# Kernel tuning notes

Hardware: AMD Instinct MI355X
Metric: run time of the kernel (lower is better)

Reference implementation:

```python
import jax, jax.numpy as jnp
import numpy as np
import math

D, H, NQP, NKP = 512, 8, 4, 4
DH = D // H
OUT_DIM = D + H * NKP * 3  # 608


def setup_inputs() -> dict:
    key = jax.random.key(0)
    ks = jax.random.split(key, 12)
    B, L = 2, 1024
    s = jax.random.normal(ks[0], (B, L, D), dtype=jnp.float32)
    R = jax.random.normal(ks[1], (B, L, 3, 3), dtype=jnp.float32)
    tr = jax.random.normal(ks[2], (B, L, 3), dtype=jnp.float32)
    sc = 0.02
    Wq = jax.random.normal(ks[3], (D, D), dtype=jnp.float32) * sc
    Wk = jax.random.normal(ks[4], (D, D), dtype=jnp.float32) * sc
    Wv = jax.random.normal(ks[5], (D, D), dtype=jnp.float32) * sc
    Wqp = jax.random.normal(ks[6], (D, H * NQP * 3), dtype=jnp.float32) * sc
    Wkp = jax.random.normal(ks[7], (D, H * NKP * 3), dtype=jnp.float32) * sc
    Wvp = jax.random.normal(ks[8], (D, H * NKP * 3), dtype=jnp.float32) * sc
    Wo = jax.random.normal(ks[9], (OUT_DIM, D), dtype=jnp.float32) * sc
    bo = jnp.zeros((D,), dtype=jnp.float32)
    gamma = jnp.ones((D,), dtype=jnp.float32)
    beta = jnp.zeros((D,), dtype=jnp.float32)
    w_C = jnp.full((H,), math.log(20.0), dtype=jnp.float32)
    return dict(s=s, R=R, tr=tr, Wq=Wq, Wk=Wk, Wv=Wv, Wqp=Wqp, Wkp=Wkp,
                Wvp=Wvp, Wo=Wo, bo=bo, gamma=gamma, beta=beta, w_C=w_C)


def _layernorm(x, gamma, beta, eps=1e-5):
    mu = jnp.mean(x, axis=-1, keepdims=True)
    var = jnp.var(x, axis=-1, keepdims=True)
    return (x - mu) * jax.lax.rsqrt(var + eps) * gamma + beta


def reference(s, R, tr, Wq, Wk, Wv, Wqp, Wkp, Wvp, Wo, bo, gamma, beta, w_C):
    B, L, _ = s.shape
    # scalar q/k/v: (B, L, H, dh)
    Q = (s @ Wq).reshape(B, L, H, DH)
    K = (s @ Wk).reshape(B, L, H, DH)
    V = (s @ Wv).reshape(B, L, H, DH)
    a_s = jnp.einsum('bihd,bjhd->bhij', Q, K) / math.sqrt(DH)
    # local points: (B, L, H, P, 3)
    Qp = (s @ Wqp).reshape(B, L, H, NQP, 3)
    Kp = (s @ Wkp).reshape(B, L, H, NKP, 3)
    Vp = (s @ Wvp).reshape(B, L, H, NKP, 3)
    tr_e = tr[:, :, None, None, :]
    to_global = lambda p: jnp.einsum('blxy,blhpy->blhpx', R, p) + tr_e
    Qp_g, Kp_g, Vp_g = to_global(Qp), to_global(Kp), to_global(Vp)
    # (B, H, L, P, 3)
    qh = jnp.transpose(Qp_g, (0, 2, 1, 3, 4))
    kh = jnp.transpose(Kp_g, (0, 2, 1, 3, 4))
    diff = qh[:, :, :, None] - kh[:, :, None]          # (B,H,L,L,P,3)
    sq_dist = jnp.sum(diff * diff, axis=(-2, -1))      # (B,H,L,L)
    wc = jax.nn.softplus(w_C)[None, :, None, None]
    attn = jax.nn.softmax(a_s - 0.5 * wc * sq_dist, axis=-1)
    out_s = jnp.einsum('bhij,bjhd->bihd', attn, V).reshape(B, L, D)
    Vp_agg = jnp.einsum('bhij,bjhpc->bihpc', attn, Vp_g)  # (B,L,H,P,3)
    # global -> local: R^T (p - tr)
    Vp_local = jnp.einsum('blyx,blhpy->blhpx', R, Vp_agg - tr_e)
    out_p = Vp_local.reshape(B, L, H * NKP * 3)
    out = jnp.concatenate([out_s, out_p], axis=-1) @ Wo + bo
    return _layernorm(s + out, gamma, beta)
```

## Files before the change

### kernel.cpp

```cpp
#include <hip/hip_runtime.h>
#include <hip/hip_fp16.h>
#include <math.h>

typedef _Float16 f16;
typedef _Float16 f16x8 __attribute__((ext_vector_type(8)));
typedef _Float16 f16x4v __attribute__((ext_vector_type(4)));
typedef float f32x4 __attribute__((ext_vector_type(4)));

#define BATCH   2
#define LSEQ    1024
#define BLTOT   2048
#define DMODEL  512
#define NHEAD   8
#define PDIM    1824
#define AW      96
#define ODIM    608
#define NSPLIT  2

__global__ __launch_bounds__(256)
void convert_s_kernel(const float* __restrict__ s, f16* __restrict__ out)
{
    const int i = blockIdx.x * 256 + threadIdx.x;
    float4 v = ((const float4*)s)[i];
    f16x4v o = { (f16)v.x, (f16)v.y, (f16)v.z, (f16)v.w };
    ((f16x4v*)out)[i] = o;
}

__global__ __launch_bounds__(256)
void transpose_wall_kernel(const float* __restrict__ Wq, const float* __restrict__ Wk,
                           const float* __restrict__ Wv, const float* __restrict__ Wqp,
                           const float* __restrict__ Wkp, const float* __restrict__ Wvp,
                           f16* __restrict__ WT)
{
    const int n0 = blockIdx.x * 32, k0 = blockIdx.y * 32;
    const int t = threadIdx.x;
    const float* src; int ld, nc0;
    if      (n0 < 512)  { src = Wq;  ld = 512; nc0 = n0; }
    else if (n0 < 1024) { src = Wk;  ld = 512; nc0 = n0 - 512; }
    else if (n0 < 1536) { src = Wv;  ld = 512; nc0 = n0 - 1024; }
    else if (n0 < 1632) { src = Wqp; ld = 96;  nc0 = n0 - 1536; }
    else if (n0 < 1728) { src = Wkp; ld = 96;  nc0 = n0 - 1632; }
    else                { src = Wvp; ld = 96;  nc0 = n0 - 1728; }

    __shared__ float tile[32][33];
#pragma unroll
    for (int i = 0; i < 4; ++i) {
        const int idx = t + i * 256;
        const int kl = idx >> 5, nl = idx & 31;
        tile[kl][nl] = src[(long long)(k0 + kl) * ld + nc0 + nl];
    }
    __syncthreads();
#pragma unroll
    for (int i = 0; i < 4; ++i) {
        const int idx = t + i * 256;
        const int nl = idx >> 5, kl = idx & 31;
        WT[(long long)(n0 + nl) * 512 + k0 + kl] = (f16)tile[kl][nl];
    }
}

__global__ __launch_bounds__(256)
void transpose_wo_kernel(const float* __restrict__ Wo, f16* __restrict__ WT)
{
    const int n0 = blockIdx.x * 32, k0 = blockIdx.y * 32;
    const int t = threadIdx.x;
    __shared__ float tile[32][33];
#pragma unroll
    for (int i = 0; i < 4; ++i) {
        const int idx = t + i * 256;
        const int kl = idx >> 5, nl = idx & 31;
        tile[kl][nl] = Wo[(long long)(k0 + kl) * 512 + n0 + nl];
    }
    __syncthreads();
#pragma unroll
    for (int i = 0; i < 4; ++i) {
        const int idx = t + i * 256;
        const int nl = idx >> 5, kl = idx & 31;
        WT[(long long)(n0 + nl) * 608 + k0 + kl] = (f16)tile[kl][nl];
    }
}

template<int BN, bool OUT16>
__global__ __launch_bounds__(256)
void gemm2_kernel(const f16* __restrict__ A, const f16* __restrict__ Bt,
                  void* __restrict__ Cout, int K, int ldc)
{
    constexpr int BCH = (BN * 4 + 255) / 256;
    __shared__ f16 As[2][64][40];
    __shared__ f16 Bs[2][BN][40];
    const int t = threadIdx.x;
    const int w = t >> 6, lane = t & 63, l15 = lane & 15, lhi = lane >> 4;
    const int row0 = blockIdx.y * 64, col0 = blockIdx.x * BN;
    const int ar = t >> 2, ac = t & 3;

    f32x4 acc[BN / 16];
#pragma unroll
    for (int n = 0; n < BN / 16; ++n) acc[n] = (f32x4){0.f, 0.f, 0.f, 0.f};

    const int nsteps = K >> 5;

    f16x8 aR;
    f16x8 bR[BCH];
    aR = *(const f16x8*)&A[(long long)(row0 + ar) * K + ac * 8];
#pragma unroll
    for (int i = 0; i < BCH; ++i) {
        const int cid = t + i * 256;
        if (cid < BN * 4) {
            const int br = cid >> 2, bc = cid & 3;
            bR[i] = *(const f16x8*)&Bt[(long long)(col0 + br) * K + bc * 8];
        }
    }
    *(f16x8*)&As[0][ar][ac * 8] = aR;
#pragma unroll
    for (int i = 0; i < BCH; ++i) {
        const int cid = t + i * 256;
        if (cid < BN * 4) *(f16x8*)&Bs[0][cid >> 2][(cid & 3) * 8] = bR[i];
    }
    __syncthreads();

    for (int st = 0; st < nsteps; ++st) {
        const int cur = st & 1;
        if (st + 1 < nsteps) {
            const int k0 = (st + 1) << 5;
            aR = *(const f16x8*)&A[(long long)(row0 + ar) * K + k0 + ac * 8];
#pragma unroll
            for (int i = 0; i < BCH; ++i) {
                const int cid = t + i * 256;
                if (cid < BN * 4) {
                    const int br = cid >> 2, bc = cid & 3;
                    bR[i] = *(const f16x8*)&Bt[(long long)(col0 + br) * K + k0 + bc * 8];
                }
            }
        }
        f16x8 af = *(const f16x8*)&As[cur][w * 16 + l15][lhi * 8];
        f16x8 bf[BN / 16];
#pragma unroll
        for (int n = 0; n < BN / 16; ++n)
            bf[n] = *(const f16x8*)&Bs[cur][n * 16 + l15][lhi * 8];
#pragma unroll
        for (int n = 0; n < BN / 16; ++n)
            acc[n] = __builtin_amdgcn_mfma_f32_16x16x32_f16(af, bf[n], acc[n], 0, 0, 0);
        if (st + 1 < nsteps) {
            *(f16x8*)&As[cur ^ 1][ar][ac * 8] = aR;
#pragma unroll
            for (int i = 0; i < BCH; ++i) {
                const int cid = t + i * 256;
                if (cid < BN * 4) *(f16x8*)&Bs[cur ^ 1][cid >> 2][(cid & 3) * 8] = bR[i];
            }
        }
        __syncthreads();
    }

    const int row = row0 + w * 16 + lhi * 4;
#pragma unroll
    for (int n = 0; n < BN / 16; ++n) {
        const int col = col0 + n * 16 + l15;
#pragma unroll
        for (int r = 0; r < 4; ++r) {
            if (OUT16) ((f16*)Cout)[(long long)(row + r) * ldc + col] = (f16)acc[n][r];
            else       ((float*)Cout)[(long long)(row + r) * ldc + col] = acc[n][r];
        }
    }
}

__global__ __launch_bounds__(256)
void build_aug_kernel(const f16* __restrict__ P, const float* __restrict__ Rm,
                      const float* __restrict__ tr, const float* __restrict__ wC,
                      f16* __restrict__ QA, f16* __restrict__ KA,
                      f16* __restrict__ VC, float* __restrict__ KOFF)
{
    const int bl = blockIdx.x;
    const int b = bl >> 10, l = bl & 1023;
    const int t = threadIdx.x;

    __shared__ float g[3][NHEAD][4][3];
    __shared__ float Rloc[9], trloc[3], wcl[NHEAD];

    if (t < 9) Rloc[t] = Rm[(long long)bl * 9 + t];
    if (t < 3) trloc[t] = tr[(long long)bl * 3 + t];
    if (t < NHEAD) { float x = wC[t]; wcl[t] = log1pf(expf(x)); }
    __syncthreads();

    const f16* Prow = P + (long long)bl * PDIM;

    if (t < 96) {
        const int proj = t / 32, tpl = t % 32, h = tpl >> 2, p = tpl & 3;
        const f16* src = Prow + 1536 + proj * 96 + h * 12 + p * 3;
        const float x = (float)src[0], y = (float)src[1], z = (float)src[2];
        g[proj][h][p][0] = Rloc[0]*x + Rloc[1]*y + Rloc[2]*z + trloc[0];
        g[proj][h][p][1] = Rloc[3]*x + Rloc[4]*y + Rloc[5]*z + trloc[1];
        g[proj][h][p][2] = Rloc[6]*x + Rloc[7]*y + Rloc[8]*z + trloc[2];
    }
    __syncthreads();

    if (t < NHEAD) {
        float s2 = 0.f;
#pragma unroll
        for (int p = 0; p < 4; ++p)
#pragma unroll
            for (int c = 0; c < 3; ++c) { float v = g[1][t][p][c]; s2 += v * v; }
        KOFF[(long long)(b * NHEAD + t) * LSEQ + l] = 0.5f * wcl[t] * s2;
    }

    for (int w = t; w < NHEAD * AW; w += 256) {
        const int h = w / AW, col = w % AW;
        const long long ro = ((long long)(b * NHEAD + h) * LSEQ + l) * AW;
        const float wc = wcl[h];
        float qv = 0.f, kv = 0.f, vv = 0.f;
        if (col < 64) {
            qv = (float)Prow[h * 64 + col] * 0.125f;
            kv = (float)Prow[512 + h * 64 + col];
            vv = (float)Prow[1024 + h * 64 + col];
        } else if (col < 76) {
            const int pc = col - 64, p = pc / 3, c = pc % 3;
            qv = wc * g[0][h][p][c];
            kv = g[1][h][p][c];
            vv = g[2][h][p][c];
        }
        QA[ro + col] = (f16)qv;
        KA[ro + col] = (f16)kv;
        VC[ro + col] = (f16)vv;
    }
}

__global__ __launch_bounds__(256)
void transpose_vct_kernel(const f16* __restrict__ VC, f16* __restrict__ VCT)
{
    const int bh = blockIdx.y, l0 = blockIdx.x * 128;
    const int t = threadIdx.x;
    __shared__ f16 tile[128][104];
#pragma unroll
    for (int i = 0; i < 6; ++i) {
        const int cid = t + i * 256;
        const int r = cid / 12, c = cid - r * 12;
        *(f16x8*)&tile[r][c * 8] =
            *(const f16x8*)&VC[((long long)bh * LSEQ + l0 + r) * AW + c * 8];
    }
    __syncthreads();
#pragma unroll
    for (int i = 0; i < 6; ++i) {
        const int cid = t + i * 256;
        const int r = cid >> 4, lg = cid & 15;
        f16x8 v;
#pragma unroll
        for (int j = 0; j < 8; ++j) v[j] = tile[lg * 8 + j][r];
        *(f16x8*)&VCT[((long long)bh * AW + r) * LSEQ + l0 + lg * 8] = v;
    }
}

__global__ __launch_bounds__(256)
void attn_kernel(const f16* __restrict__ QA, const f16* __restrict__ KA,
                 const f16* __restrict__ VCT, const float* __restrict__ KOFF,
                 float* __restrict__ OCp, float2* __restrict__ ML)
{
    const int bh = blockIdx.y;
    const int q0 = blockIdx.x * 64;
    const int z  = blockIdx.z;
    const int t = threadIdx.x;
    const int w = t >> 6, lane = t & 63, l15 = lane & 15, lhi = lane >> 4;

    __shared__ f16 Ks[128][104];
    __shared__ f16 Vs[96][136];
    __shared__ f16 Ps[64][136];

    const f16* qbase = QA + ((long long)bh * LSEQ + q0 + w * 16 + l15) * AW;
    f16x8 qf[3];
#pragma unroll
    for (int ks = 0; ks < 3; ++ks)
        qf[ks] = *(const f16x8*)(qbase + ks * 32 + lhi * 8);

    f32x4 Oacc[6];
#pragma unroll
    for (int nv = 0; nv < 6; ++nv) Oacc[nv] = (f32x4){0.f, 0.f, 0.f, 0.f};
    float M[4], L[4];
#pragma unroll
    for (int r = 0; r < 4; ++r) { M[r] = -1e30f; L[r] = 0.f; }

    const f16* kgbase = KA + (long long)bh * LSEQ * AW;
    const f16* vgbase = VCT + (long long)bh * AW * LSEQ;
    const float* koffb = KOFF + (long long)bh * LSEQ;

    const int kvbeg = z * (LSEQ / NSPLIT);
    const int kvend = kvbeg + LSEQ / NSPLIT;

    for (int kv0 = kvbeg; kv0 < kvend; kv0 += 128) {
#pragma unroll
        for (int i = 0; i < 6; ++i) {
            const int cid = t + i * 256;
            const int r = cid / 12, c = cid - r * 12;
            *(f16x8*)&Ks[r][c * 8] = *(const f16x8*)(kgbase + (long long)(kv0 + r) * AW + c * 8);
        }
#pragma unroll
        for (int i = 0; i < 6; ++i) {
            const int cid = t + i * 256;
            const int r = cid >> 4, c = cid & 15;
            *(f16x8*)&Vs[r][c * 8] = *(const f16x8*)(vgbase + (long long)r * LSEQ + kv0 + c * 8);
        }
        __syncthreads();

        f32x4 sc[8];
#pragma unroll
        for (int n = 0; n < 8; ++n) sc[n] = (f32x4){0.f, 0.f, 0.f, 0.f};
        __builtin_amdgcn_s_setprio(1);
#pragma unroll
        for (int n = 0; n < 8; ++n)
#pragma unroll
            for (int ks = 0; ks < 3; ++ks) {
                f16x8 kb = *(const f16x8*)&Ks[n * 16 + l15][ks * 32 + lhi * 8];
                sc[n] = __builtin_amdgcn_mfma_f32_16x16x32_f16(qf[ks], kb, sc[n], 0, 0, 0);
            }
        __builtin_amdgcn_s_setprio(0);
#pragma unroll
        for (int n = 0; n < 8; ++n) {
            const float ko = koffb[kv0 + n * 16 + l15];
#pragma unroll
            for (int r = 0; r < 4; ++r) sc[n][r] -= ko;
        }
        float sscale[4];
#pragma unroll
        for (int r = 0; r < 4; ++r) {
            float mr = sc[0][r];
#pragma unroll
            for (int n = 1; n < 8; ++n) mr = fmaxf(mr, sc[n][r]);
#pragma unroll
            for (int off = 1; off < 16; off <<= 1) mr = fmaxf(mr, __shfl_xor(mr, off));
            const float nm = fmaxf(M[r], mr);
            sscale[r] = __expf(M[r] - nm);
            M[r] = nm;
        }
        float rsum[4] = {0.f, 0.f, 0.f, 0.f};
#pragma unroll
        for (int n = 0; n < 8; ++n)
#pragma unroll
            for (int r = 0; r < 4; ++r) {
                const float p = __expf(sc[n][r] - M[r]);
                sc[n][r] = p;
                rsum[r] += p;
            }
#pragma unroll
        for (int r = 0; r < 4; ++r) {
            float s = rsum[r];
#pragma unroll
            for (int off = 1; off < 16; off <<= 1) s += __shfl_xor(s, off);
            L[r] = L[r] * sscale[r] + s;
        }
#pragma unroll
        for (int nv = 0; nv < 6; ++nv)
#pragma unroll
            for (int r = 0; r < 4; ++r) Oacc[nv][r] *= sscale[r];

#pragma unroll
        for (int n = 0; n < 8; ++n)
#pragma unroll
            for (int r = 0; r < 4; ++r)
                Ps[w * 16 + lhi * 4 + r][n * 16 + l15] = (f16)sc[n][r];

        f16x8 pa[4];
#pragma unroll
        for (int ks = 0; ks < 4; ++ks)
            pa[ks] = *(const f16x8*)&Ps[w * 16 + l15][ks * 32 + lhi * 8];
        __builtin_amdgcn_s_setprio(1);
#pragma unroll
        for (int nv = 0; nv < 6; ++nv)
#pragma unroll
            for (int ks = 0; ks < 4; ++ks) {
                f16x8 vb = *(const f16x8*)&Vs[nv * 16 + l15][ks * 32 + lhi * 8];
                Oacc[nv] = __builtin_amdgcn_mfma_f32_16x16x32_f16(pa[ks], vb, Oacc[nv], 0, 0, 0);
            }
        __builtin_amdgcn_s_setprio(0);
        __syncthreads();
    }

    float* obase = OCp + (((long long)(z * 16 + bh) * LSEQ) + q0 + w * 16 + lhi * 4) * AW;
#pragma unroll
    for (int nv = 0; nv < 6; ++nv)
#pragma unroll
        for (int r = 0; r < 4; ++r)
            obase[r * AW + nv * 16 + l15] = Oacc[nv][r];
    if (l15 == 0) {
#pragma unroll
        for (int r = 0; r < 4; ++r)
            ML[(long long)(z * 16 + bh) * LSEQ + q0 + w * 16 + lhi * 4 + r] =
                make_float2(M[r], L[r]);
    }
}

__global__ __launch_bounds__(256)
void combine_concat_kernel(const float* __restrict__ OCp, const float2* __restrict__ ML,
                           const float* __restrict__ Rm, const float* __restrict__ tr,
                           f16* __restrict__ CC)
{
    const int bl = blockIdx.x;
    const int b = bl >> 10, l = bl & 1023;
    const int t = threadIdx.x;

    __shared__ float w1[8], w2[8];
    __shared__ float o[8][AW];
    __shared__ float Rloc[9], trloc[3];
    if (t < 9) Rloc[t] = Rm[(long long)bl * 9 + t];
    if (t < 3) trloc[t] = tr[(long long)bl * 3 + t];
    if (t < 8) {
        const int bh = b * 8 + t;
        const float2 m1 = ML[(long long)bh * LSEQ + l];
        const float2 m2 = ML[(long long)(16 + bh) * LSEQ + l];
        const float mm = fmaxf(m1.x, m2.x);
        const float e1 = __expf(m1.x - mm), e2 = __expf(m2.x - mm);
        const float inv = 1.0f / (m1.y * e1 + m2.y * e2);
        w1[t] = e1 * inv; w2[t] = e2 * inv;
    }
    __syncthreads();
    for (int idx = t; idx < 8 * AW; idx += 256) {
        const int h = idx / AW, c = idx - h * AW;
        const float* p1 = OCp + ((long long)(b * 8 + h) * LSEQ + l) * AW;
        const float* p2 = OCp + ((long long)(16 + b * 8 + h) * LSEQ + l) * AW;
        o[h][c] = p1[c] * w1[h] + p2[c] * w2[h];
    }
    __syncthreads();

    f16* crow = CC + (long long)bl * ODIM;
    for (int c = t; c < DMODEL; c += 256) crow[c] = (f16)o[c >> 6][c & 63];
    if (t < 32) {
        const int h = t >> 2, p = t & 3;
        const float x = o[h][64 + p * 3 + 0] - trloc[0];
        const float y = o[h][64 + p * 3 + 1] - trloc[1];
        const float z = o[h][64 + p * 3 + 2] - trloc[2];
        crow[512 + h * 12 + p * 3 + 0] = (f16)(Rloc[0]*x + Rloc[3]*y + Rloc[6]*z);
        crow[512 + h * 12 + p * 3 + 1] = (f16)(Rloc[1]*x + Rloc[4]*y + Rloc[7]*z);
        crow[512 + h * 12 + p * 3 + 2] = (f16)(Rloc[2]*x + Rloc[5]*y + Rloc[8]*z);
    }
}

__global__ __launch_bounds__(256)
void residual_ln_kernel(const float* __restrict__ s, const float* __restrict__ Y,
                        const float* __restrict__ bo, const float* __restrict__ gamma,
                        const float* __restrict__ beta, float* __restrict__ out)
{
    const int bl = blockIdx.x;
    const int t = threadIdx.x;
    const float* srow = s + (long long)bl * DMODEL;
    const float* yrow = Y + (long long)bl * DMODEL;

    const float v0 = srow[t]       + yrow[t]       + bo[t];
    const float v1 = srow[t + 256] + yrow[t + 256] + bo[t + 256];

    float sum = v0 + v1, sq = v0 * v0 + v1 * v1;
#pragma unroll
    for (int o = 32; o > 0; o >>= 1) {
        sum += __shfl_xor(sum, o);
        sq  += __shfl_xor(sq,  o);
    }
    __shared__ float rs[4], rq[4];
    const int wid = t >> 6, lane = t & 63;
    if (lane == 0) { rs[wid] = sum; rq[wid] = sq; }
    __syncthreads();
    sum = rs[0] + rs[1] + rs[2] + rs[3];
    sq  = rq[0] + rq[1] + rq[2] + rq[3];

    const float mu  = sum * (1.0f / DMODEL);
    const float var = sq * (1.0f / DMODEL) - mu * mu;
    const float inv = rsqrtf(var + 1e-5f);

    out[(long long)bl * DMODEL + t]       = (v0 - mu) * inv * gamma[t]       + beta[t];
    out[(long long)bl * DMODEL + t + 256] = (v1 - mu) * inv * gamma[t + 256] + beta[t + 256];
}

extern "C" void kernel_launch(void* const* d_in, const int* in_sizes, int n_in,
                              void* d_out, int out_size, void* d_ws, size_t ws_size,
                              hipStream_t stream)
{
    const float* s    = (const float*)d_in[0];
    const float* R    = (const float*)d_in[1];
    const float* tr   = (const float*)d_in[2];
    const float* Wq   = (const float*)d_in[3];
    const float* Wk   = (const float*)d_in[4];
    const float* Wv   = (const float*)d_in[5];
    const float* Wqp  = (const float*)d_in[6];
    const float* Wkp  = (const float*)d_in[7];
    const float* Wvp  = (const float*)d_in[8];
    const float* Wo   = (const float*)d_in[9];
    const float* bo   = (const float*)d_in[10];
    const float* gam  = (const float*)d_in[11];
    const float* bet  = (const float*)d_in[12];
    const float* wC   = (const float*)d_in[13];
    float* out = (float*)d_out;

    f16* sH    = (f16*)d_ws;
    f16* WallT = sH + 1048576;
    f16* WoT   = WallT + 933888;
    f16* P     = WoT + 311296;
    f16* QA    = P + 3735552;
    f16* KA    = QA + 1572864;
    f16* VC    = KA + 1572864;
    f16* VCT   = VC + 1572864;
    float* KOFF = (float*)(VCT + 1572864);
    float* OCp  = KOFF + 16384;
    float2* ML  = (float2*)(OCp + 3145728);
    f16* CC     = (f16*)(ML + 32768);
    float* Y    = (float*)(CC + 1245184);

    const dim3 blk(256);

    convert_s_kernel<<<dim3(1024), blk, 0, stream>>>(s, sH);
    transpose_wall_kernel<<<dim3(57, 16), blk, 0, stream>>>(Wq, Wk, Wv, Wqp, Wkp, Wvp, WallT);
    transpose_wo_kernel<<<dim3(16, 19), blk, 0, stream>>>(Wo, WoT);

    gemm2_kernel<96, true><<<dim3(19, 32), blk, 0, stream>>>(sH, WallT, P, 512, 1824);

    build_aug_kernel<<<dim3(BLTOT), blk, 0, stream>>>(P, R, tr, wC, QA, KA, VC, KOFF);
    transpose_vct_kernel<<<dim3(8, 16), blk, 0, stream>>>(VC, VCT);

    attn_kernel<<<dim3(16, 16, NSPLIT), blk, 0, stream>>>(QA, KA, VCT, KOFF, OCp, ML);

    combine_concat_kernel<<<dim3(BLTOT), blk, 0, stream>>>(OCp, ML, R, tr, CC);

    gemm2_kernel<64, false><<<dim3(8, 32), blk, 0, stream>>>(CC, WoT, Y, 608, 512);

    residual_ln_kernel<<<dim3(BLTOT), blk, 0, stream>>>(s, Y, bo, gam, bet, out);
}
```

Before: 79.57 us.

## Merge prep kernels, fuse build and V transpose, prefetch KV, fp16 partials

Merges the s conversion and both weight transposes into one prep kernel. Replaces the per-row build_aug and separate V transpose with a per-(batch, head, 64-row) tile kernel that writes QA/KA with vector stores and VCT directly through shared memory. In attention, the next K/V tile is register-prefetched while the current tile is computed, launch_bounds is raised to 2 blocks per SM, and the split-KV partial outputs are stored as fp16. This removes launches and intermediate traffic, at the cost of more register pressure and lower precision in the partial outputs.

```diff
diff --git a/kernel.cpp b/kernel.cpp
--- a/kernel.cpp
+++ b/kernel.cpp
@@ -18,64 +18,65 @@
 #define NSPLIT  2
 
 __global__ __launch_bounds__(256)
-void convert_s_kernel(const float* __restrict__ s, f16* __restrict__ out)
-{
-    const int i = blockIdx.x * 256 + threadIdx.x;
-    float4 v = ((const float4*)s)[i];
-    f16x4v o = { (f16)v.x, (f16)v.y, (f16)v.z, (f16)v.w };
-    ((f16x4v*)out)[i] = o;
-}
-
-__global__ __launch_bounds__(256)
-void transpose_wall_kernel(const float* __restrict__ Wq, const float* __restrict__ Wk,
-                           const float* __restrict__ Wv, const float* __restrict__ Wqp,
-                           const float* __restrict__ Wkp, const float* __restrict__ Wvp,
-                           f16* __restrict__ WT)
-{
-    const int n0 = blockIdx.x * 32, k0 = blockIdx.y * 32;
-    const int t = threadIdx.x;
-    const float* src; int ld, nc0;
-    if      (n0 < 512)  { src = Wq;  ld = 512; nc0 = n0; }
-    else if (n0 < 1024) { src = Wk;  ld = 512; nc0 = n0 - 512; }
-    else if (n0 < 1536) { src = Wv;  ld = 512; nc0 = n0 - 1024; }
-    else if (n0 < 1632) { src = Wqp; ld = 96;  nc0 = n0 - 1536; }
-    else if (n0 < 1728) { src = Wkp; ld = 96;  nc0 = n0 - 1632; }
-    else                { src = Wvp; ld = 96;  nc0 = n0 - 1728; }
-
-    __shared__ float tile[32][33];
-#pragma unroll
-    for (int i = 0; i < 4; ++i) {
-        const int idx = t + i * 256;
-        const int kl = idx >> 5, nl = idx & 31;
-        tile[kl][nl] = src[(long long)(k0 + kl) * ld + nc0 + nl];
-    }
-    __syncthreads();
-#pragma unroll
-    for (int i = 0; i < 4; ++i) {
-        const int idx = t + i * 256;
-        const int nl = idx >> 5, kl = idx & 31;
-        WT[(long long)(n0 + nl) * 512 + k0 + kl] = (f16)tile[kl][nl];
-    }
-}
-
-__global__ __launch_bounds__(256)
-void transpose_wo_kernel(const float* __restrict__ Wo, f16* __restrict__ WT)
-{
-    const int n0 = blockIdx.x * 32, k0 = blockIdx.y * 32;
+void prep_kernel(const float* __restrict__ s,
+                 const float* __restrict__ Wq, const float* __restrict__ Wk,
+                 const float* __restrict__ Wv, const float* __restrict__ Wqp,
+                 const float* __restrict__ Wkp, const float* __restrict__ Wvp,
+                 const float* __restrict__ Wo,
+                 f16* __restrict__ sH, f16* __restrict__ WallT, f16* __restrict__ WoT)
+{
+    const int blk = blockIdx.x;
     const int t = threadIdx.x;
     __shared__ float tile[32][33];
-#pragma unroll
-    for (int i = 0; i < 4; ++i) {
-        const int idx = t + i * 256;
-        const int kl = idx >> 5, nl = idx & 31;
-        tile[kl][nl] = Wo[(long long)(k0 + kl) * 512 + n0 + nl];
-    }
-    __syncthreads();
-#pragma unroll
-    for (int i = 0; i < 4; ++i) {
-        const int idx = t + i * 256;
-        const int nl = idx >> 5, kl = idx & 31;
-        WT[(long long)(n0 + nl) * 608 + k0 + kl] = (f16)tile[kl][nl];
+
+    if (blk < 1024) {
+        const int i = blk * 256 + t;
+        float4 v = ((const float4*)s)[i];
+        f16x4v o = { (f16)v.x, (f16)v.y, (f16)v.z, (f16)v.w };
+        ((f16x4v*)sH)[i] = o;
+        return;
+    }
+    if (blk < 1936) {
+        const int idx = blk - 1024;
+        const int n0 = (idx % 57) * 32, k0 = (idx / 57) * 32;
+        const float* src; int ld, nc0;
+        if      (n0 < 512)  { src = Wq;  ld = 512; nc0 = n0; }
+        else if (n0 < 1024) { src = Wk;  ld = 512; nc0 = n0 - 512; }
+        else if (n0 < 1536) { src = Wv;  ld = 512; nc0 = n0 - 1024; }
+        else if (n0 < 1632) { src = Wqp; ld = 96;  nc0 = n0 - 1536; }
+        else if (n0 < 1728) { src = Wkp; ld = 96;  nc0 = n0 - 1632; }
+        else                { src = Wvp; ld = 96;  nc0 = n0 - 1728; }
+#pragma unroll
+        for (int i = 0; i < 4; ++i) {
+            const int idx2 = t + i * 256;
+            const int kl = idx2 >> 5, nl = idx2 & 31;
+            tile[kl][nl] = src[(long long)(k0 + kl) * ld + nc0 + nl];
+        }
+        __syncthreads();
+#pragma unroll
+        for (int i = 0; i < 4; ++i) {
+            const int idx2 = t + i * 256;
+            const int nl = idx2 >> 5, kl = idx2 & 31;
+            WallT[(long long)(n0 + nl) * 512 + k0 + kl] = (f16)tile[kl][nl];
+        }
+        return;
+    }
+    {
+        const int idx = blk - 1936;
+        const int n0 = (idx % 16) * 32, k0 = (idx / 16) * 32;
+#pragma unroll
+        for (int i = 0; i < 4; ++i) {
+            const int idx2 = t + i * 256;
+            const int kl = idx2 >> 5, nl = idx2 & 31;
+            tile[kl][nl] = Wo[(long long)(k0 + kl) * 512 + n0 + nl];
+        }
+        __syncthreads();
+#pragma unroll
+        for (int i = 0; i < 4; ++i) {
+            const int idx2 = t + i * 256;
+            const int nl = idx2 >> 5, kl = idx2 & 31;
+            WoT[(long long)(n0 + nl) * 608 + k0 + kl] = (f16)tile[kl][nl];
+        }
     }
 }
 
@@ -163,94 +164,108 @@
 }
 
 __global__ __launch_bounds__(256)
-void build_aug_kernel(const f16* __restrict__ P, const float* __restrict__ Rm,
-                      const float* __restrict__ tr, const float* __restrict__ wC,
-                      f16* __restrict__ QA, f16* __restrict__ KA,
-                      f16* __restrict__ VC, float* __restrict__ KOFF)
-{
-    const int bl = blockIdx.x;
-    const int b = bl >> 10, l = bl & 1023;
+void build_aug2_kernel(const f16* __restrict__ P, const float* __restrict__ Rm,
+                       const float* __restrict__ tr, const float* __restrict__ wC,
+                       f16* __restrict__ QA, f16* __restrict__ KA,
+                       f16* __restrict__ VCT, float* __restrict__ KOFF)
+{
+    const int l0 = blockIdx.x * 64;
+    const int bh = blockIdx.y;
+    const int b = bh >> 3, h = bh & 7;
     const int t = threadIdx.x;
 
-    __shared__ float g[3][NHEAD][4][3];
-    __shared__ float Rloc[9], trloc[3], wcl[NHEAD];
-
-    if (t < 9) Rloc[t] = Rm[(long long)bl * 9 + t];
-    if (t < 3) trloc[t] = tr[(long long)bl * 3 + t];
-    if (t < NHEAD) { float x = wC[t]; wcl[t] = log1pf(expf(x)); }
-    __syncthreads();
-
-    const f16* Prow = P + (long long)bl * PDIM;
-
-    if (t < 96) {
-        const int proj = t / 32, tpl = t % 32, h = tpl >> 2, p = tpl & 3;
-        const f16* src = Prow + 1536 + proj * 96 + h * 12 + p * 3;
+    __shared__ float Rl[64][9];
+    __shared__ float trl[64][3];
+    __shared__ f16 gq[64][12];
+    __shared__ f16 gk[64][12];
+    __shared__ float k2[64][4];
+    __shared__ f16 Vt[96][72];
+    __shared__ float wcs;
+
+    const long long blbase = (long long)b * LSEQ + l0;
+
+    for (int i = t; i < 64 * 9; i += 256) Rl[i / 9][i % 9] = Rm[blbase * 9 + i];
+    for (int i = t; i < 64 * 3; i += 256) trl[i / 3][i % 3] = tr[blbase * 3 + i];
+    if (t == 0) { float x = wC[h]; wcs = log1pf(expf(x)); }
+    __syncthreads();
+    const float wc = wcs;
+
+    for (int i = t; i < 768; i += 256) {
+        const int l = i / 12, pp = i - l * 12;
+        const int proj = pp >> 2, p = pp & 3;
+        const f16* src = P + (blbase + l) * PDIM + 1536 + proj * 96 + h * 12 + p * 3;
         const float x = (float)src[0], y = (float)src[1], z = (float)src[2];
-        g[proj][h][p][0] = Rloc[0]*x + Rloc[1]*y + Rloc[2]*z + trloc[0];
-        g[proj][h][p][1] = Rloc[3]*x + Rloc[4]*y + Rloc[5]*z + trloc[1];
-        g[proj][h][p][2] = Rloc[6]*x + Rloc[7]*y + Rloc[8]*z + trloc[2];
-    }
-    __syncthreads();
-
-    if (t < NHEAD) {
-        float s2 = 0.f;
-#pragma unroll
-        for (int p = 0; p < 4; ++p)
-#pragma unroll
-            for (int c = 0; c < 3; ++c) { float v = g[1][t][p][c]; s2 += v * v; }
-        KOFF[(long long)(b * NHEAD + t) * LSEQ + l] = 0.5f * wcl[t] * s2;
-    }
-
-    for (int w = t; w < NHEAD * AW; w += 256) {
-        const int h = w / AW, col = w % AW;
-        const long long ro = ((long long)(b * NHEAD + h) * LSEQ + l) * AW;
-        const float wc = wcl[h];
-        float qv = 0.f, kv = 0.f, vv = 0.f;
-        if (col < 64) {
-            qv = (float)Prow[h * 64 + col] * 0.125f;
-            kv = (float)Prow[512 + h * 64 + col];
-            vv = (float)Prow[1024 + h * 64 + col];
-        } else if (col < 76) {
-            const int pc = col - 64, p = pc / 3, c = pc % 3;
-            qv = wc * g[0][h][p][c];
-            kv = g[1][h][p][c];
-            vv = g[2][h][p][c];
-        }
-        QA[ro + col] = (f16)qv;
-        KA[ro + col] = (f16)kv;
-        VC[ro + col] = (f16)vv;
-    }
-}
-
-__global__ __launch_bounds__(256)
-void transpose_vct_kernel(const f16* __restrict__ VC, f16* __restrict__ VCT)
-{
-    const int bh = blockIdx.y, l0 = blockIdx.x * 128;
-    const int t = threadIdx.x;
-    __shared__ f16 tile[128][104];
-#pragma unroll
-    for (int i = 0; i < 6; ++i) {
-        const int cid = t + i * 256;
-        const int r = cid / 12, c = cid - r * 12;
-        *(f16x8*)&tile[r][c * 8] =
-            *(const f16x8*)&VC[((long long)bh * LSEQ + l0 + r) * AW + c * 8];
-    }
-    __syncthreads();
-#pragma unroll
-    for (int i = 0; i < 6; ++i) {
-        const int cid = t + i * 256;
-        const int r = cid >> 4, lg = cid & 15;
-        f16x8 v;
-#pragma unroll
-        for (int j = 0; j < 8; ++j) v[j] = tile[lg * 8 + j][r];
-        *(f16x8*)&VCT[((long long)bh * AW + r) * LSEQ + l0 + lg * 8] = v;
-    }
-}
-
-__global__ __launch_bounds__(256)
+        const float gx = Rl[l][0]*x + Rl[l][1]*y + Rl[l][2]*z + trl[l][0];
+        const float gy = Rl[l][3]*x + Rl[l][4]*y + Rl[l][5]*z + trl[l][1];
+        const float gz = Rl[l][6]*x + Rl[l][7]*y + Rl[l][8]*z + trl[l][2];
+        if (proj == 0) {
+            gq[l][p * 3 + 0] = (f16)(wc * gx);
+            gq[l][p * 3 + 1] = (f16)(wc * gy);
+            gq[l][p * 3 + 2] = (f16)(wc * gz);
+        } else if (proj == 1) {
+            gk[l][p * 3 + 0] = (f16)gx;
+            gk[l][p * 3 + 1] = (f16)gy;
+            gk[l][p * 3 + 2] = (f16)gz;
+            k2[l][p] = gx * gx + gy * gy + gz * gz;
+        } else {
+            Vt[64 + p * 3 + 0][l] = (f16)gx;
+            Vt[64 + p * 3 + 1][l] = (f16)gy;
+            Vt[64 + p * 3 + 2][l] = (f16)gz;
+        }
+    }
+    for (int i = t; i < 512; i += 256) {
+        const int l = i >> 3, ch = i & 7;
+        f16x8 v = *(const f16x8*)&P[(blbase + l) * PDIM + 1024 + h * 64 + ch * 8];
+#pragma unroll
+        for (int j = 0; j < 8; ++j) Vt[ch * 8 + j][l] = v[j];
+    }
+    for (int i = t; i < 180; i += 256) {
+        const int r = 76 + i / 9, ch = i % 9;
+        *(f16x8*)&Vt[r][ch * 8] = (f16x8){0,0,0,0,0,0,0,0};
+    }
+    __syncthreads();
+
+    if (t < 64)
+        KOFF[(long long)bh * LSEQ + l0 + t] =
+            0.5f * wc * (k2[t][0] + k2[t][1] + k2[t][2] + k2[t][3]);
+
+    for (int i = t; i < 768; i += 256) {
+        const int l = i / 12, ch = i - l * 12;
+        const long long prow = (blbase + l) * PDIM;
+        const long long orow = ((long long)bh * LSEQ + l0 + l) * AW;
+        f16x8 q, k;
+        if (ch < 8) {
+            f16x8 qv = *(const f16x8*)&P[prow + h * 64 + ch * 8];
+            f16x8 kv = *(const f16x8*)&P[prow + 512 + h * 64 + ch * 8];
+            q = qv * (f16)0.125f;
+            k = kv;
+        } else if (ch == 8) {
+#pragma unroll
+            for (int j = 0; j < 8; ++j) { q[j] = gq[l][j]; k[j] = gk[l][j]; }
+        } else if (ch == 9) {
+#pragma unroll
+            for (int j = 0; j < 8; ++j) {
+                q[j] = (j < 4) ? gq[l][8 + j] : (f16)0.f;
+                k[j] = (j < 4) ? gk[l][8 + j] : (f16)0.f;
+            }
+        } else {
+            q = (f16x8){0,0,0,0,0,0,0,0};
+            k = (f16x8){0,0,0,0,0,0,0,0};
+        }
+        *(f16x8*)&QA[orow + ch * 8] = q;
+        *(f16x8*)&KA[orow + ch * 8] = k;
+    }
+    for (int i = t; i < 768; i += 256) {
+        const int c = i >> 3, lg = i & 7;
+        *(f16x8*)&VCT[((long long)bh * AW + c) * LSEQ + l0 + lg * 8] =
+            *(const f16x8*)&Vt[c][lg * 8];
+    }
+}
+
+__global__ __launch_bounds__(256, 2)
 void attn_kernel(const f16* __restrict__ QA, const f16* __restrict__ KA,
                  const f16* __restrict__ VCT, const float* __restrict__ KOFF,
-                 float* __restrict__ OCp, float2* __restrict__ ML)
+                 f16* __restrict__ OCp, float2* __restrict__ ML)
 {
     const int bh = blockIdx.y;
     const int q0 = blockIdx.x * 64;
@@ -282,20 +297,37 @@
     const int kvbeg = z * (LSEQ / NSPLIT);
     const int kvend = kvbeg + LSEQ / NSPLIT;
 
+#pragma unroll
+    for (int i = 0; i < 6; ++i) {
+        const int cid = t + i * 256;
+        const int r = cid / 12, c = cid - r * 12;
+        *(f16x8*)&Ks[r][c * 8] = *(const f16x8*)(kgbase + (long long)(kvbeg + r) * AW + c * 8);
+    }
+#pragma unroll
+    for (int i = 0; i < 6; ++i) {
+        const int cid = t + i * 256;
+        const int r = cid >> 4, c = cid & 15;
+        *(f16x8*)&Vs[r][c * 8] = *(const f16x8*)(vgbase + (long long)r * LSEQ + kvbeg + c * 8);
+    }
+    __syncthreads();
+
     for (int kv0 = kvbeg; kv0 < kvend; kv0 += 128) {
-#pragma unroll
-        for (int i = 0; i < 6; ++i) {
-            const int cid = t + i * 256;
-            const int r = cid / 12, c = cid - r * 12;
-            *(f16x8*)&Ks[r][c * 8] = *(const f16x8*)(kgbase + (long long)(kv0 + r) * AW + c * 8);
-        }
-#pragma unroll
-        for (int i = 0; i < 6; ++i) {
-            const int cid = t + i * 256;
-            const int r = cid >> 4, c = cid & 15;
-            *(f16x8*)&Vs[r][c * 8] = *(const f16x8*)(vgbase + (long long)r * LSEQ + kv0 + c * 8);
-        }
-        __syncthreads();
+        const bool more = (kv0 + 128 < kvend);
+        f16x8 kpre[6], vpre[6];
+        if (more) {
+#pragma unroll
+            for (int i = 0; i < 6; ++i) {
+                const int cid = t + i * 256;
+                const int r = cid / 12, c = cid - r * 12;
+                kpre[i] = *(const f16x8*)(kgbase + (long long)(kv0 + 128 + r) * AW + c * 8);
+            }
+#pragma unroll
+            for (int i = 0; i < 6; ++i) {
+                const int cid = t + i * 256;
+                const int r = cid >> 4, c = cid & 15;
+                vpre[i] = *(const f16x8*)(vgbase + (long long)r * LSEQ + kv0 + 128 + c * 8);
+            }
+        }
 
         f32x4 sc[8];
 #pragma unroll
@@ -368,14 +400,30 @@
             }
         __builtin_amdgcn_s_setprio(0);
         __syncthreads();
-    }
-
-    float* obase = OCp + (((long long)(z * 16 + bh) * LSEQ) + q0 + w * 16 + lhi * 4) * AW;
+
+        if (more) {
+#pragma unroll
+            for (int i = 0; i < 6; ++i) {
+                const int cid = t + i * 256;
+                const int r = cid / 12, c = cid - r * 12;
+                *(f16x8*)&Ks[r][c * 8] = kpre[i];
+            }
+#pragma unroll
+            for (int i = 0; i < 6; ++i) {
+                const int cid = t + i * 256;
+                const int r = cid >> 4, c = cid & 15;
+                *(f16x8*)&Vs[r][c * 8] = vpre[i];
+            }
+        }
+        __syncthreads();
+    }
+
+    f16* obase = OCp + (((long long)(z * 16 + bh) * LSEQ) + q0 + w * 16 + lhi * 4) * AW;
 #pragma unroll
     for (int nv = 0; nv < 6; ++nv)
 #pragma unroll
         for (int r = 0; r < 4; ++r)
-            obase[r * AW + nv * 16 + l15] = Oacc[nv][r];
+            obase[r * AW + nv * 16 + l15] = (f16)Oacc[nv][r];
     if (l15 == 0) {
 #pragma unroll
         for (int r = 0; r < 4; ++r)
@@ -385,7 +433,7 @@
 }
 
 __global__ __launch_bounds__(256)
-void combine_concat_kernel(const float* __restrict__ OCp, const float2* __restrict__ ML,
+void combine_concat_kernel(const f16* __restrict__ OCp, const float2* __restrict__ ML,
                            const float* __restrict__ Rm, const float* __restrict__ tr,
                            f16* __restrict__ CC)
 {
@@ -410,9 +458,9 @@
     __syncthreads();
     for (int idx = t; idx < 8 * AW; idx += 256) {
         const int h = idx / AW, c = idx - h * AW;
-        const float* p1 = OCp + ((long long)(b * 8 + h) * LSEQ + l) * AW;
-        const float* p2 = OCp + ((long long)(16 + b * 8 + h) * LSEQ + l) * AW;
-        o[h][c] = p1[c] * w1[h] + p2[c] * w2[h];
+        const f16* p1 = OCp + ((long long)(b * 8 + h) * LSEQ + l) * AW;
+        const f16* p2 = OCp + ((long long)(16 + b * 8 + h) * LSEQ + l) * AW;
+        o[h][c] = (float)p1[c] * w1[h] + (float)p2[c] * w2[h];
     }
     __syncthreads();
 
@@ -489,24 +537,21 @@
     f16* P     = WoT + 311296;
     f16* QA    = P + 3735552;
     f16* KA    = QA + 1572864;
-    f16* VC    = KA + 1572864;
-    f16* VCT   = VC + 1572864;
+    f16* VCT   = KA + 1572864;
     float* KOFF = (float*)(VCT + 1572864);
-    float* OCp  = KOFF + 16384;
+    f16* OCp    = (f16*)(KOFF + 16384);
     float2* ML  = (float2*)(OCp + 3145728);
     f16* CC     = (f16*)(ML + 32768);
     float* Y    = (float*)(CC + 1245184);
 
     const dim3 blk(256);
 
-    convert_s_kernel<<<dim3(1024), blk, 0, stream>>>(s, sH);
-    transpose_wall_kernel<<<dim3(57, 16), blk, 0, stream>>>(Wq, Wk, Wv, Wqp, Wkp, Wvp, WallT);
-    transpose_wo_kernel<<<dim3(16, 19), blk, 0, stream>>>(Wo, WoT);
+    prep_kernel<<<dim3(2240), blk, 0, stream>>>(s, Wq, Wk, Wv, Wqp, Wkp, Wvp, Wo,
+                                                sH, WallT, WoT);
 
     gemm2_kernel<96, true><<<dim3(19, 32), blk, 0, stream>>>(sH, WallT, P, 512, 1824);
 
-    build_aug_kernel<<<dim3(BLTOT), blk, 0, stream>>>(P, R, tr, wC, QA, KA, VC, KOFF);
-    transpose_vct_kernel<<<dim3(8, 16), blk, 0, stream>>>(VC, VCT);
+    build_aug2_kernel<<<dim3(16, 16), blk, 0, stream>>>(P, R, tr, wC, QA, KA, VCT, KOFF);
 
     attn_kernel<<<dim3(16, 16, NSPLIT), blk, 0, stream>>>(QA, KA, VCT, KOFF, OCp, ML);
 
```

Result: faster. 72.90 us (-8.4%).
